# Kernel optimization log

Measured on AMD Instinct MI355X. Metric: run time of the kernel, lower is better.

## Reference

```python
import jax, jax.numpy as jnp
import numpy as np

B, S, H, D = 4, 2048, 12, 64
HID = H * D  # 768
EPS = 1e-5


def _layer_norm(h, w, b):
    mu = jnp.mean(h, axis=-1, keepdims=True)
    var = jnp.mean((h - mu) ** 2, axis=-1, keepdims=True)
    return w * (h - mu) / jnp.sqrt(var + EPS) + b


def setup_inputs() -> dict:
    key = jax.random.key(0)
    ks = jax.random.split(key, 12)
    sc = 1.0 / np.sqrt(HID)
    inp = {
        "x": jax.random.normal(ks[0], (B, S, HID), jnp.float32),
        "ln1_w": jnp.ones((HID,), jnp.float32),
        "ln1_b": jnp.zeros((HID,), jnp.float32),
        "Wq": jax.random.normal(ks[1], (HID, HID), jnp.float32) * sc,
        "bq": jnp.zeros((HID,), jnp.float32),
        "Wk": jax.random.normal(ks[2], (HID, HID), jnp.float32) * sc,
        "bk": jnp.zeros((HID,), jnp.float32),
        "Wv": jax.random.normal(ks[3], (HID, HID), jnp.float32) * sc,
        "bv": jnp.zeros((HID,), jnp.float32),
        "Wo": jax.random.normal(ks[4], (HID, HID), jnp.float32) * sc,
        "bo": jnp.zeros((HID,), jnp.float32),
        "ln2_w": jnp.ones((HID,), jnp.float32),
        "ln2_b": jnp.zeros((HID,), jnp.float32),
        "W1": jax.random.normal(ks[5], (HID, 4 * HID), jnp.float32) * sc,
        "b1": jnp.zeros((4 * HID,), jnp.float32),
        "W2": jax.random.normal(ks[6], (4 * HID, HID), jnp.float32) * (1.0 / np.sqrt(4 * HID)),
        "b2": jnp.zeros((HID,), jnp.float32),
    }
    return inp


def _split_heads(t):
    # (B, S, H*D) -> (B, H, S, D)
    b, s, _ = t.shape
    return t.reshape(b, s, H, -1).transpose(0, 2, 1, 3)


def _merge_heads(t):
    # (B, H, S, D) -> (B, S, H*D)
    b, h, s, d = t.shape
    return t.transpose(0, 2, 1, 3).reshape(b, s, h * d)


def _attention(h, Wq, bq, Wk, bk, Wv, bv, Wo, bo):
    q = _split_heads(h @ Wq + bq)  # (B,H,S,D)
    k = _split_heads(h @ Wk + bk)
    v = _split_heads(h @ Wv + bv)
    scores = jnp.einsum("bhqd,bhkd->bhqk", q, k) / jnp.sqrt(jnp.asarray(D, h.dtype))
    causal = jnp.tril(jnp.ones((q.shape[2], q.shape[2]), bool))  # (S,S)
    scores = jnp.where(causal, scores, jnp.finfo(scores.dtype).min)
    w = jax.nn.softmax(scores, axis=-1)
    out = jnp.einsum("bhqk,bhkd->bhqd", w, v)
    return _merge_heads(out) @ Wo + bo


def reference(x, ln1_w, ln1_b, Wq, bq, Wk, bk, Wv, bv, Wo, bo, ln2_w, ln2_b, W1, b1, W2, b2):
    # Pre-LN transformer block: x + attn(LN(x)); then x + MLP(LN(x))
    a = _attention(_layer_norm(x, ln1_w, ln1_b), Wq, bq, Wk, bk, Wv, bv, Wo, bo)
    x = x + a
    h = _layer_norm(x, ln2_w, ln2_b)
    m = jax.nn.gelu(h @ W1 + b1, approximate=False) @ W2 + b2
    return x + m
```

## Files before the change

### kernel.cpp

```cpp
#include <hip/hip_runtime.h>
#include <cmath>
#include <stdint.h>

typedef unsigned short u16;
typedef __attribute__((ext_vector_type(8))) short short8;
typedef __attribute__((ext_vector_type(4))) float f32x4;
typedef __attribute__((ext_vector_type(4))) unsigned int u32x4;

#define HID 768
#define FF  3072
#define SEQ 2048
#define NHEAD 12
#define NROWS 8192

__device__ __forceinline__ float bf2f(u16 u){ return __uint_as_float(((unsigned)u)<<16); }
__device__ __forceinline__ u16 f2bf(float f){
  unsigned x = __float_as_uint(f);
  x += 0x7fffu + ((x>>16)&1u);
  return (u16)(x>>16);
}
__device__ __forceinline__ void gload16(const void* g, void* l){
  __builtin_amdgcn_global_load_lds((const __attribute__((address_space(1))) unsigned*)g,
                                   (__attribute__((address_space(3))) unsigned*)l, 16, 0, 0);
}

__global__ __launch_bounds__(256) void wconv(const float* __restrict__ in,
                                             u16* __restrict__ out, int K, int N)
{
  __shared__ float t[32][33];
  const int bk = blockIdx.x*32, bn = blockIdx.y*32;
  const int tn = threadIdx.x & 31, tk = threadIdx.x >> 5;
  #pragma unroll
  for (int j=0;j<4;++j)
    t[tk+8*j][tn] = in[(size_t)(bk+tk+8*j)*N + bn + tn];
  __syncthreads();
  #pragma unroll
  for (int j=0;j<4;++j)
    out[(size_t)(bn+tk+8*j)*K + bk + tn] = f2bf(t[tn][tk+8*j]);
}

__global__ __launch_bounds__(256) void ln_k(const float* __restrict__ in,
    const float* __restrict__ gw, const float* __restrict__ gb,
    u16* __restrict__ out)
{
  const int row = blockIdx.x*4 + (threadIdx.x>>6);
  const int l = threadIdx.x & 63;
  const float* p = in + (size_t)row*HID;
  float4 v[3];
  float s=0.f, ss=0.f;
  #pragma unroll
  for (int j=0;j<3;++j){
    v[j] = *(const float4*)(p + j*256 + l*4);
    s  += v[j].x + v[j].y + v[j].z + v[j].w;
    ss += v[j].x*v[j].x + v[j].y*v[j].y + v[j].z*v[j].z + v[j].w*v[j].w;
  }
  #pragma unroll
  for (int m=1;m<64;m<<=1){
    s  += __shfl_xor(s,  m, 64);
    ss += __shfl_xor(ss, m, 64);
  }
  const float mu = s * (1.f/768.f);
  const float rstd = rsqrtf(ss*(1.f/768.f) - mu*mu + 1e-5f);
  #pragma unroll
  for (int j=0;j<3;++j){
    const float4 wv = *(const float4*)(gw + j*256 + l*4);
    const float4 bv = *(const float4*)(gb + j*256 + l*4);
    ushort4 o;
    o.x = f2bf((v[j].x-mu)*rstd*wv.x + bv.x);
    o.y = f2bf((v[j].y-mu)*rstd*wv.y + bv.y);
    o.z = f2bf((v[j].z-mu)*rstd*wv.z + bv.z);
    o.w = f2bf((v[j].w-mu)*rstd*wv.w + bv.w);
    *(ushort4*)(out + (size_t)row*HID + j*256 + l*4) = o;
  }
}

template<int MODE>
__global__ __launch_bounds__(256) void gemm_bt(const u16* __restrict__ A,
    const u16* __restrict__ Bt, const float* __restrict__ bias0,
    const float* __restrict__ bias1, const float* __restrict__ bias2,
    const float* __restrict__ res, void* __restrict__ outp,
    int N, int K, long wstride, long ostride)
{
  __shared__ __align__(16) u16 sA[128*32];
  __shared__ __align__(16) u16 sB[128*32];
  const int tid = threadIdx.x, l = tid&63, w = tid>>6;
  const int wr = w>>1, wc = w&1, hi = l>>4, lo = l&15;
  const int bm = blockIdx.x*128, bn = blockIdx.y*128;
  const int z = blockIdx.z;
  const u16* Bz = Bt + (size_t)z * (size_t)wstride;
  const float* bias = (z==0) ? bias0 : ((z==1)? bias1 : bias2);

  const f32x4 zv = {0.f,0.f,0.f,0.f};
  f32x4 acc[4][4];
  #pragma unroll
  for (int i=0;i<4;++i)
    #pragma unroll
    for (int j=0;j<4;++j) acc[i][j] = zv;

  for (int kt=0; kt<K; kt+=32){
    __syncthreads();
    #pragma unroll
    for (int j=0;j<2;++j){
      int c = tid + 256*j;
      int row = c>>2, off = (c&3)*8;
      gload16(A  + (size_t)(bm + row)*K + kt + off, (char*)sA + c*16);
      gload16(Bz + (size_t)(bn + row)*K + kt + off, (char*)sB + c*16);
    }
    __syncthreads();
    short8 af[4], bfv[4];
    #pragma unroll
    for (int i=0;i<4;++i){
      af[i]  = *(const short8*)(sA + (wr*64 + i*16 + lo)*32 + hi*8);
      bfv[i] = *(const short8*)(sB + (wc*64 + i*16 + lo)*32 + hi*8);
    }
    #pragma unroll
    for (int mi=0;mi<4;++mi)
      #pragma unroll
      for (int ni=0;ni<4;++ni)
        acc[mi][ni] = __builtin_amdgcn_mfma_f32_16x16x32_bf16(af[mi], bfv[ni], acc[mi][ni], 0,0,0);
  }

  #pragma unroll
  for (int mi=0;mi<4;++mi)
    #pragma unroll
    for (int ni=0;ni<4;++ni){
      const int r0 = bm + wr*64 + mi*16 + 4*hi;
      const int cc = bn + wc*64 + ni*16 + lo;
      const float bv = bias[cc];
      #pragma unroll
      for (int g=0; g<4; ++g){
        const size_t idx = (size_t)(r0+g)*N + cc;
        float v = acc[mi][ni][g] + bv;
        if (MODE == 0){
          ((u16*)outp + (size_t)z*(size_t)ostride)[idx] = f2bf(v);
        } else if (MODE == 1){
          ((float*)outp)[idx] = res[idx] + v;
        } else {
          float gx = 0.5f*v*(1.f + erff(v*0.70710678118f));
          ((u16*)outp)[idx] = f2bf(gx);
        }
      }
    }
}

__global__ __launch_bounds__(256, 4) void attn_k(const u16* __restrict__ Qm,
                                                 const u16* __restrict__ Km,
                                                 const u16* __restrict__ Vm,
                                                 u16* __restrict__ Om)
{
  __shared__ __align__(16) u16 sK[64*64];
  __shared__ __align__(16) u16 sV[64*72];
  __shared__ __align__(16) u16 sP[4][16*72];
  const int tid = threadIdx.x, l = tid & 63, w = tid >> 6;
  const int hi = l >> 4, lo = l & 15;
  const int idx = blockIdx.x;
  const int qb = 31 - (idx / 48);
  const int bh = idx % 48;
  const int b = bh / NHEAD, h = bh - (bh / NHEAD) * NHEAD;
  const size_t rb = (size_t)b * SEQ;
  const int qw = qb*64 + w*16;

  short8 qf[2];
  #pragma unroll
  for (int ks=0; ks<2; ++ks){
    short8 t = *(const short8*)(Qm + (rb + qw + lo)*HID + h*64 + ks*32 + hi*8);
    #pragma unroll
    for (int i=0;i<8;++i) t[i] = (short)f2bf(bf2f((u16)t[i]) * 0.125f);
    qf[ks] = t;
  }

  const f32x4 zv = {0.f,0.f,0.f,0.f};
  f32x4 oa[4] = {zv, zv, zv, zv};
  float m = -INFINITY, lsum = 0.f;
  u16* pw = sP[w];

  for (int t=0; t<=qb; ++t){
    const int kv0 = t*64;
    __syncthreads();
    #pragma unroll
    for (int j=0;j<2;++j){
      int c = tid + 256*j;
      int row = c >> 3, off = (c&7)*8;
      gload16(Km + (rb + kv0 + row)*HID + h*64 + off, (char*)sK + c*16);
    }
    #pragma unroll
    for (int j=0;j<2;++j){
      int c = tid + 256*j;
      int row = c >> 3, d0 = (c&7)*8;
      u32x4 raw = *(const u32x4*)(Vm + (rb + kv0 + row)*HID + h*64 + d0);
      #pragma unroll
      for (int i=0;i<8;++i){
        u16 uu = (u16)((raw[i>>1] >> ((i&1)*16)) & 0xffffu);
        sV[(d0+i)*72 + row] = uu;
      }
    }
    __syncthreads();

    f32x4 sc[4] = {zv, zv, zv, zv};
    #pragma unroll
    for (int ks=0;ks<2;++ks){
      #pragma unroll
      for (int ni=0;ni<4;++ni){
        short8 kf = *(const short8*)(sK + (ni*16 + lo)*64 + ks*32 + hi*8);
        sc[ni] = __builtin_amdgcn_mfma_f32_16x16x32_bf16(kf, qf[ks], sc[ni], 0,0,0);
      }
    }

    if (t == qb){
      #pragma unroll
      for (int ni=0;ni<4;++ni)
        #pragma unroll
        for (int g=0; g<4; ++g){
          int kg = kv0 + ni*16 + 4*hi + g;
          if (kg > qw + lo) sc[ni][g] = -INFINITY;
        }
    }

    float pm = sc[0][0];
    #pragma unroll
    for (int ni=0;ni<4;++ni)
      #pragma unroll
      for (int g=0; g<4; ++g) pm = fmaxf(pm, sc[ni][g]);
    pm = fmaxf(pm, __shfl_xor(pm, 16, 64));
    pm = fmaxf(pm, __shfl_xor(pm, 32, 64));
    const float mnew = fmaxf(m, pm);
    const float alpha = __expf(m - mnew);
    float ps = 0.f;
    #pragma unroll
    for (int ni=0;ni<4;++ni)
      #pragma unroll
      for (int g=0; g<4; ++g){
        float e = __expf(sc[ni][g] - mnew);
        sc[ni][g] = e;
        ps += e;
      }
    ps += __shfl_xor(ps, 16, 64);
    ps += __shfl_xor(ps, 32, 64);
    lsum = lsum*alpha + ps;
    m = mnew;
    #pragma unroll
    for (int nd=0;nd<4;++nd){
      oa[nd][0]*=alpha; oa[nd][1]*=alpha; oa[nd][2]*=alpha; oa[nd][3]*=alpha;
    }

    #pragma unroll
    for (int ni=0;ni<4;++ni)
      #pragma unroll
      for (int g=0; g<4; ++g)
        pw[lo*72 + ni*16 + 4*hi + g] = f2bf(sc[ni][g]);
    asm volatile("" ::: "memory");

    #pragma unroll
    for (int ks=0;ks<2;++ks){
      short8 pb = *(const short8*)(pw + lo*72 + ks*32 + hi*8);
      #pragma unroll
      for (int nd=0;nd<4;++nd){
        short8 vf = *(const short8*)(sV + (nd*16 + lo)*72 + ks*32 + hi*8);
        oa[nd] = __builtin_amdgcn_mfma_f32_16x16x32_bf16(vf, pb, oa[nd], 0,0,0);
      }
    }
  }

  const float inv = 1.f / lsum;
  #pragma unroll
  for (int nd=0;nd<4;++nd){
    ushort4 o;
    o.x = f2bf(oa[nd][0]*inv);
    o.y = f2bf(oa[nd][1]*inv);
    o.z = f2bf(oa[nd][2]*inv);
    o.w = f2bf(oa[nd][3]*inv);
    *(ushort4*)(Om + (rb + qw + lo)*HID + h*64 + nd*16 + 4*hi) = o;
  }
}

extern "C" void kernel_launch(void* const* d_in, const int* in_sizes, int n_in,
                              void* d_out, int out_size, void* d_ws, size_t ws_size,
                              hipStream_t stream)
{
  const float* x    = (const float*)d_in[0];
  const float* ln1w = (const float*)d_in[1];
  const float* ln1b = (const float*)d_in[2];
  const float* Wq   = (const float*)d_in[3];
  const float* bq   = (const float*)d_in[4];
  const float* Wk   = (const float*)d_in[5];
  const float* bk   = (const float*)d_in[6];
  const float* Wv   = (const float*)d_in[7];
  const float* bv   = (const float*)d_in[8];
  const float* Wo   = (const float*)d_in[9];
  const float* bo   = (const float*)d_in[10];
  const float* ln2w = (const float*)d_in[11];
  const float* ln2b = (const float*)d_in[12];
  const float* W1   = (const float*)d_in[13];
  const float* b1   = (const float*)d_in[14];
  const float* W2   = (const float*)d_in[15];
  const float* b2   = (const float*)d_in[16];

  u16* wq_t = (u16*)d_ws;
  u16* wk_t = wq_t + 589824;
  u16* wv_t = wk_t + 589824;
  u16* wo_t = wv_t + 589824;
  u16* w1_t = wo_t + 589824;
  u16* w2_t = w1_t + 2359296;
  u16* hbf  = w2_t + 2359296;
  u16* qb_  = hbf + 6291456;
  u16* kb_  = qb_ + 6291456;
  u16* vb_  = kb_ + 6291456;
  u16* atb  = vb_ + 6291456;
  u16* ub   = qb_;
  float* x2 = (float*)(atb + 6291456);

  const size_t need = 102236160ull;
  if (ws_size < need) return;

  dim3 blk(256);
  wconv<<<dim3(24,24), blk, 0, stream>>>(Wq, wq_t, 768, 768);
  wconv<<<dim3(24,24), blk, 0, stream>>>(Wk, wk_t, 768, 768);
  wconv<<<dim3(24,24), blk, 0, stream>>>(Wv, wv_t, 768, 768);
  wconv<<<dim3(24,24), blk, 0, stream>>>(Wo, wo_t, 768, 768);
  wconv<<<dim3(24,96), blk, 0, stream>>>(W1, w1_t, 768, 3072);
  wconv<<<dim3(96,24), blk, 0, stream>>>(W2, w2_t, 3072, 768);

  ln_k<<<2048, blk, 0, stream>>>(x, ln1w, ln1b, hbf);

  gemm_bt<0><<<dim3(64,6,3), blk, 0, stream>>>(hbf, wq_t, bq, bk, bv,
      nullptr, (void*)qb_, 768, 768, 589824L, 6291456L);

  attn_k<<<dim3(1536), blk, 0, stream>>>(qb_, kb_, vb_, atb);

  gemm_bt<1><<<dim3(64,6,1), blk, 0, stream>>>(atb, wo_t, bo, bo, bo,
      x, (void*)x2, 768, 768, 0L, 0L);

  ln_k<<<2048, blk, 0, stream>>>(x2, ln2w, ln2b, hbf);

  gemm_bt<2><<<dim3(64,24,1), blk, 0, stream>>>(hbf, w1_t, b1, b1, b1,
      nullptr, (void*)ub, 3072, 768, 0L, 0L);

  gemm_bt<1><<<dim3(64,6,1), blk, 0, stream>>>(ub, w2_t, b2, b2, b2,
      x2, d_out, 768, 3072, 0L, 0L);
}
```

Measured before the change: 472.5 us.

## Pre-transpose V, swizzle K/V shared tiles, pass P via shuffles

V is now computed by a separate GEMM launch and transposed into a (HID, NROWS) bf16 buffer by a new tconv kernel, which reuses the hbf scratch. Attention can then fill its V tile with async global-to-LDS loads instead of scalar transposing stores. K and V^T tiles use an XOR swizzle to avoid LDS bank conflicts. The probability tile is repacked with cross-lane shuffles rather than a round trip through shared memory. In exchange it adds an extra transpose pass over V and one more kernel launch.

Result: faster. 432.6 us (-8.4%).

```diff
diff --git a/kernel.cpp b/kernel.cpp
--- a/kernel.cpp
+++ b/kernel.cpp
@@ -19,6 +19,9 @@
   x += 0x7fffu + ((x>>16)&1u);
   return (u16)(x>>16);
 }
+__device__ __forceinline__ unsigned pack2(float a, float b){
+  return (unsigned)f2bf(a) | ((unsigned)f2bf(b) << 16);
+}
 __device__ __forceinline__ void gload16(const void* g, void* l){
   __builtin_amdgcn_global_load_lds((const __attribute__((address_space(1))) unsigned*)g,
                                    (__attribute__((address_space(3))) unsigned*)l, 16, 0, 0);
@@ -37,6 +40,21 @@
   #pragma unroll
   for (int j=0;j<4;++j)
     out[(size_t)(bn+tk+8*j)*K + bk + tn] = f2bf(t[tn][tk+8*j]);
+}
+
+__global__ __launch_bounds__(256) void tconv(const u16* __restrict__ in,
+                                             u16* __restrict__ out, int K, int N)
+{
+  __shared__ u16 t[32][34];
+  const int bk = blockIdx.x*32, bn = blockIdx.y*32;
+  const int tn = threadIdx.x & 31, tk = threadIdx.x >> 5;
+  #pragma unroll
+  for (int j=0;j<4;++j)
+    t[tk+8*j][tn] = in[(size_t)(bk+tk+8*j)*N + bn + tn];
+  __syncthreads();
+  #pragma unroll
+  for (int j=0;j<4;++j)
+    out[(size_t)(bn+tk+8*j)*K + bk + tn] = t[tn][tk+8*j];
 }
 
 __global__ __launch_bounds__(256) void ln_k(const float* __restrict__ in,
@@ -145,12 +163,11 @@
 
 __global__ __launch_bounds__(256, 4) void attn_k(const u16* __restrict__ Qm,
                                                  const u16* __restrict__ Km,
-                                                 const u16* __restrict__ Vm,
+                                                 const u16* __restrict__ Vt,
                                                  u16* __restrict__ Om)
 {
-  __shared__ __align__(16) u16 sK[64*64];
-  __shared__ __align__(16) u16 sV[64*72];
-  __shared__ __align__(16) u16 sP[4][16*72];
+  __shared__ __align__(16) u16 sK [64*64];
+  __shared__ __align__(16) u16 sVT[64*64];
   const int tid = threadIdx.x, l = tid & 63, w = tid >> 6;
   const int hi = l >> 4, lo = l & 15;
   const int idx = blockIdx.x;
@@ -172,7 +189,8 @@
   const f32x4 zv = {0.f,0.f,0.f,0.f};
   f32x4 oa[4] = {zv, zv, zv, zv};
   float m = -INFINITY, lsum = 0.f;
-  u16* pw = sP[w];
+  const int srcA = (((2*hi)  & 3) << 4) | lo;
+  const int srcB = (((2*hi+1)& 3) << 4) | lo;
 
   for (int t=0; t<=qb; ++t){
     const int kv0 = t*64;
@@ -180,19 +198,16 @@
     #pragma unroll
     for (int j=0;j<2;++j){
       int c = tid + 256*j;
-      int row = c >> 3, off = (c&7)*8;
-      gload16(Km + (rb + kv0 + row)*HID + h*64 + off, (char*)sK + c*16);
+      int row = c >> 3;
+      int d0 = ((c&7) ^ (row&7))*8;
+      gload16(Km + (rb + kv0 + row)*HID + h*64 + d0, (char*)sK + c*16);
     }
     #pragma unroll
     for (int j=0;j<2;++j){
       int c = tid + 256*j;
-      int row = c >> 3, d0 = (c&7)*8;
-      u32x4 raw = *(const u32x4*)(Vm + (rb + kv0 + row)*HID + h*64 + d0);
-      #pragma unroll
-      for (int i=0;i<8;++i){
-        u16 uu = (u16)((raw[i>>1] >> ((i&1)*16)) & 0xffffu);
-        sV[(d0+i)*72 + row] = uu;
-      }
+      int row = c >> 3;
+      int k0 = ((c&7) ^ (row&7))*8;
+      gload16(Vt + (size_t)(h*64 + row)*NROWS + rb + kv0 + k0, (char*)sVT + c*16);
     }
     __syncthreads();
 
@@ -201,7 +216,7 @@
     for (int ks=0;ks<2;++ks){
       #pragma unroll
       for (int ni=0;ni<4;++ni){
-        short8 kf = *(const short8*)(sK + (ni*16 + lo)*64 + ks*32 + hi*8);
+        short8 kf = *(const short8*)(sK + (ni*16 + lo)*64 + ((ks*32 + hi*8) ^ ((lo&7)*8)));
         sc[ni] = __builtin_amdgcn_mfma_f32_16x16x32_bf16(kf, qf[ks], sc[ni], 0,0,0);
       }
     }
@@ -244,19 +259,26 @@
     }
 
     #pragma unroll
-    for (int ni=0;ni<4;++ni)
-      #pragma unroll
-      for (int g=0; g<4; ++g)
-        pw[lo*72 + ni*16 + 4*hi + g] = f2bf(sc[ni][g]);
-    asm volatile("" ::: "memory");
-
-    #pragma unroll
     for (int ks=0;ks<2;++ks){
-      short8 pb = *(const short8*)(pw + lo*72 + ks*32 + hi*8);
+      unsigned pkA0 = pack2(sc[2*ks  ][0], sc[2*ks  ][1]);
+      unsigned pkA1 = pack2(sc[2*ks  ][2], sc[2*ks  ][3]);
+      unsigned pkB0 = pack2(sc[2*ks+1][0], sc[2*ks+1][1]);
+      unsigned pkB1 = pack2(sc[2*ks+1][2], sc[2*ks+1][3]);
+      unsigned a0 = (unsigned)__shfl((int)pkA0, srcA, 64);
+      unsigned b0 = (unsigned)__shfl((int)pkB0, srcA, 64);
+      unsigned a1 = (unsigned)__shfl((int)pkA1, srcA, 64);
+      unsigned b1 = (unsigned)__shfl((int)pkB1, srcA, 64);
+      unsigned a2 = (unsigned)__shfl((int)pkA0, srcB, 64);
+      unsigned b2 = (unsigned)__shfl((int)pkB0, srcB, 64);
+      unsigned a3 = (unsigned)__shfl((int)pkA1, srcB, 64);
+      unsigned b3 = (unsigned)__shfl((int)pkB1, srcB, 64);
+      union { u32x4 u; short8 s; } pf;
+      pf.u = (u32x4){ (hi<2)?a0:b0, (hi<2)?a1:b1, (hi<2)?a2:b2, (hi<2)?a3:b3 };
+
       #pragma unroll
       for (int nd=0;nd<4;++nd){
-        short8 vf = *(const short8*)(sV + (nd*16 + lo)*72 + ks*32 + hi*8);
-        oa[nd] = __builtin_amdgcn_mfma_f32_16x16x32_bf16(vf, pb, oa[nd], 0,0,0);
+        short8 vf = *(const short8*)(sVT + (nd*16 + lo)*64 + ((ks*32 + hi*8) ^ ((lo&7)*8)));
+        oa[nd] = __builtin_amdgcn_mfma_f32_16x16x32_bf16(vf, pf.s, oa[nd], 0,0,0);
       }
     }
   }
@@ -322,10 +344,13 @@
 
   ln_k<<<2048, blk, 0, stream>>>(x, ln1w, ln1b, hbf);
 
-  gemm_bt<0><<<dim3(64,6,3), blk, 0, stream>>>(hbf, wq_t, bq, bk, bv,
+  gemm_bt<0><<<dim3(64,6,2), blk, 0, stream>>>(hbf, wq_t, bq, bk, bv,
       nullptr, (void*)qb_, 768, 768, 589824L, 6291456L);
-
-  attn_k<<<dim3(1536), blk, 0, stream>>>(qb_, kb_, vb_, atb);
+  gemm_bt<0><<<dim3(64,6,1), blk, 0, stream>>>(hbf, wv_t, bv, bv, bv,
+      nullptr, (void*)vb_, 768, 768, 0L, 0L);
+  tconv<<<dim3(256,24), blk, 0, stream>>>(vb_, hbf, 8192, 768);
+
+  attn_k<<<dim3(1536), blk, 0, stream>>>(qb_, kb_, hbf, atb);
 
   gemm_bt<1><<<dim3(64,6,1), blk, 0, stream>>>(atb, wo_t, bo, bo, bo,
       x, (void*)x2, 768, 768, 0L, 0L);
```
